# Performance work log

Hardware: AMD Instinct MI355X
Metric: run time of the kernel (lower is better)

The kernel has to match this reference:

```python
import jax, jax.numpy as jnp
import numpy as np

INF = 1.0e9
B, NI, NJ = 1, 768, 768
C_NODE, C_PAIR = 512, 128
H, C_HID = 8, 32
LN_EPS = 1e-5


def _ln(x, w, b):
    m = jnp.mean(x, axis=-1, keepdims=True)
    v = jnp.mean(jnp.square(x - m), axis=-1, keepdims=True)
    return (x - m) * jax.lax.rsqrt(v + LN_EPS) * w + b


def setup_inputs() -> dict:
    key = jax.random.key(0)
    ks = jax.random.split(key, 16)
    s_node = 1.0 / np.sqrt(C_NODE)
    s_pair = 1.0 / np.sqrt(C_PAIR)
    s_hid = 1.0 / np.sqrt(H * C_HID)
    inp = {
        "node_embed_i": jax.random.normal(ks[0], (B, NI, C_NODE), jnp.float32),
        "node_embed_j": jax.random.normal(ks[1], (B, NJ, C_NODE), jnp.float32),
        "pair_embed": jax.random.normal(ks[2], (B, NI, NJ, C_PAIR), jnp.float32),
        "pair_mask": (jax.random.uniform(ks[3], (B, NI, NJ)) < 0.95).astype(jnp.float32),
        "node_mask_i": (jax.random.uniform(ks[4], (B, NI)) < 0.98).astype(jnp.float32),
        # LayerNorm params
        "ln_i_w": jnp.ones((C_NODE,), jnp.float32), "ln_i_b": jnp.zeros((C_NODE,), jnp.float32),
        "ln_j_w": jnp.ones((C_NODE,), jnp.float32), "ln_j_b": jnp.zeros((C_NODE,), jnp.float32),
        "ln_p_w": jnp.ones((C_PAIR,), jnp.float32), "ln_p_b": jnp.zeros((C_PAIR,), jnp.float32),
        # pair-bias projection and its gate: Linear(C_PAIR, H)
        "W_pb": jax.random.normal(ks[5], (C_PAIR, H), jnp.float32) * s_pair,
        "b_pb": jnp.zeros((H,), jnp.float32),
        "W_pg": jax.random.normal(ks[6], (C_PAIR, H), jnp.float32) * s_pair,
        "b_pg": jnp.zeros((H,), jnp.float32),
        # attention projections (q/k/v bias-free, OpenFold-style)
        "Wq": jax.random.normal(ks[7], (C_NODE, H * C_HID), jnp.float32) * s_node,
        "Wk": jax.random.normal(ks[8], (C_NODE, H * C_HID), jnp.float32) * s_node,
        "Wv": jax.random.normal(ks[9], (C_NODE, H * C_HID), jnp.float32) * s_node,
        # output gate and output projection
        "Wg": jax.random.normal(ks[10], (C_NODE, H * C_HID), jnp.float32) * s_node,
        "bg": jnp.zeros((H * C_HID,), jnp.float32),
        "Wo": jax.random.normal(ks[11], (H * C_HID, C_NODE), jnp.float32) * s_hid,
        "bo": jnp.zeros((C_NODE,), jnp.float32),
    }
    return inp


def reference(node_embed_i, node_embed_j, pair_embed, pair_mask, node_mask_i,
              ln_i_w, ln_i_b, ln_j_w, ln_j_b, ln_p_w, ln_p_b,
              W_pb, b_pb, W_pg, b_pg, Wq, Wk, Wv, Wg, bg, Wo, bo):
    # LayerNorms
    qx = _ln(node_embed_i, ln_i_w, ln_i_b)           # [B,NI,C_NODE]
    kx = _ln(node_embed_j, ln_j_w, ln_j_b)           # [B,NJ,C_NODE]
    p = _ln(pair_embed, ln_p_w, ln_p_b)              # [B,NI,NJ,C_PAIR]

    # additive mask bias: 0 where valid, -inf where masked; broadcast over heads
    mask_bias = (INF * (pair_mask - 1.0))[:, None, :, :]          # [B,1,NI,NJ]

    # gated pair bias -> [B,H,NI,NJ] (permute_final_dims([2,0,1]))
    pb = (p @ W_pb + b_pb) * jax.nn.sigmoid(p @ W_pg + b_pg)      # [B,NI,NJ,H]
    pair_bias = jnp.transpose(pb, (0, 3, 1, 2))

    # multi-head attention with injected biases
    q = (qx @ Wq).reshape(B, NI, H, C_HID) * (C_HID ** -0.5)
    k = (kx @ Wk).reshape(B, NJ, H, C_HID)
    v = (kx @ Wv).reshape(B, NJ, H, C_HID)
    scores = jnp.einsum('bihc,bjhc->bhij', q, k) + mask_bias + pair_bias
    a = jax.nn.softmax(scores, axis=-1)                           # [B,H,NI,NJ]
    o = jnp.einsum('bhij,bjhc->bihc', a, v)                       # [B,NI,H,C_HID]

    # sigmoid output gate, flatten heads, output projection
    g = jax.nn.sigmoid(qx @ Wg + bg).reshape(B, NI, H, C_HID)
    o = (o * g).reshape(B, NI, H * C_HID)
    mha_out = o @ Wo + bo                                         # [B,NI,C_NODE]

    # residual on the layernormed input, scaled by node mask (dropout = identity at inference)
    return qx + mha_out * node_mask_i[..., None]
```

## Files before the change

kernel.cpp:

```cpp
#include <hip/hip_runtime.h>
#include <hip/hip_bf16.h>

#define NI 768
#define NJ 768
#define CN 512
#define CP 128
#define NH 8
#define CH 32
#define HC 256

typedef float  fx4  __attribute__((ext_vector_type(4)));
typedef float  fx2  __attribute__((ext_vector_type(2)));
typedef short  bv8  __attribute__((ext_vector_type(8)));
typedef unsigned short usx4 __attribute__((ext_vector_type(4)));

__device__ __forceinline__ short f2bf(float f) {
    __hip_bfloat16 h = __float2bfloat16(f);
    return *reinterpret_cast<short*>(&h);
}
__device__ __forceinline__ float bf2f(unsigned short u) {
    union { unsigned int u; float f; } c; c.u = ((unsigned int)u) << 16; return c.f;
}

__global__ __launch_bounds__(256) void fused_front_kernel(
    const float* __restrict__ node_i, const float* __restrict__ node_j,
    const float* __restrict__ ln_i_w, const float* __restrict__ ln_i_b,
    const float* __restrict__ ln_j_w, const float* __restrict__ ln_j_b,
    const float* __restrict__ Wq, const float* __restrict__ Wk,
    const float* __restrict__ Wv, const float* __restrict__ Wg,
    const float* __restrict__ bg,
    const float* __restrict__ lnpw, const float* __restrict__ lnpb,
    const float* __restrict__ Wpb, const float* __restrict__ bpb,
    const float* __restrict__ Wpg, const float* __restrict__ bpg,
    const float* __restrict__ pair, const float* __restrict__ pmask,
    float* __restrict__ qx, unsigned short* __restrict__ qsb,
    unsigned short* __restrict__ ksb, unsigned short* __restrict__ vtb,
    float* __restrict__ gs, unsigned short* __restrict__ biasb)
{
    const int bid = blockIdx.x;
    const int t = threadIdx.x;
    if (bid < 192) {
        __shared__ float xs[8][CN];
        __shared__ float red[4][8][2];
        const bool isj = bid >= 96;
        const int r0 = (isj ? bid - 96 : bid) * 8;
        const float* xin = isj ? node_j : node_i;
        const float* lw = isj ? ln_j_w : ln_i_w;
        const float* lb = isj ? ln_j_b : ln_i_b;
        const int wv = t >> 6;

        fx2 vrow[8]; float s8[8], q8[8];
#pragma unroll
        for (int r = 0; r < 8; ++r) {
            vrow[r] = *(const fx2*)(xin + (size_t)(r0 + r) * CN + t * 2);
            s8[r] = vrow[r][0] + vrow[r][1];
            q8[r] = vrow[r][0] * vrow[r][0] + vrow[r][1] * vrow[r][1];
        }
#pragma unroll
        for (int d = 1; d < 64; d <<= 1)
#pragma unroll
            for (int r = 0; r < 8; ++r) {
                s8[r] += __shfl_xor(s8[r], d);
                q8[r] += __shfl_xor(q8[r], d);
            }
        if ((t & 63) == 0)
#pragma unroll
            for (int r = 0; r < 8; ++r) { red[wv][r][0] = s8[r]; red[wv][r][1] = q8[r]; }
        __syncthreads();
        fx2 lwv = *(const fx2*)(lw + t * 2), lbv = *(const fx2*)(lb + t * 2);
#pragma unroll
        for (int r = 0; r < 8; ++r) {
            float s = red[0][r][0] + red[1][r][0] + red[2][r][0] + red[3][r][0];
            float q = red[0][r][1] + red[1][r][1] + red[2][r][1] + red[3][r][1];
            float mean = s * (1.f / CN);
            float var = q * (1.f / CN) - mean * mean;
            float rs = rsqrtf(var + 1e-5f);
            fx2 o;
            o[0] = (vrow[r][0] - mean) * rs * lwv[0] + lbv[0];
            o[1] = (vrow[r][1] - mean) * rs * lwv[1] + lbv[1];
            xs[r][t * 2] = o[0]; xs[r][t * 2 + 1] = o[1];
            if (!isj) *(fx2*)(qx + (size_t)(r0 + r) * CN + t * 2) = o;
        }
        __syncthreads();

        for (int m = 0; m < 2; ++m) {
            const float* W = isj ? (m ? Wv : Wk) : (m ? Wg : Wq);
            float acc[8] = {0.f,0.f,0.f,0.f,0.f,0.f,0.f,0.f};
            for (int cc = 0; cc < CN; cc += 4) {
                fx4 xv[8];
#pragma unroll
                for (int r = 0; r < 8; ++r) xv[r] = *(const fx4*)&xs[r][cc];
#pragma unroll
                for (int u = 0; u < 4; ++u) {
                    float w = W[(size_t)(cc + u) * HC + t];
#pragma unroll
                    for (int r = 0; r < 8; ++r) acc[r] = fmaf(xv[r][u], w, acc[r]);
                }
            }
            if (!isj) {
                if (m == 0) {
#pragma unroll
                    for (int r = 0; r < 8; ++r)
                        qsb[(size_t)(r0 + r) * HC + t] =
                            (unsigned short)f2bf(acc[r] * 0.17677669529663687f);
                } else {
#pragma unroll
                    for (int r = 0; r < 8; ++r)
                        gs[(size_t)(r0 + r) * HC + t] =
                            1.f / (1.f + __expf(-(acc[r] + bg[t])));
                }
            } else {
                if (m == 0) {
#pragma unroll
                    for (int r = 0; r < 8; ++r)
                        ksb[(size_t)(r0 + r) * HC + t] = (unsigned short)f2bf(acc[r]);
                } else {
                    bv8 vv;
#pragma unroll
                    for (int r = 0; r < 8; ++r) vv[r] = f2bf(acc[r]);
                    *(bv8*)&vtb[(size_t)t * NJ + r0] = vv;
                }
            }
        }
        return;
    }

    __shared__ unsigned short wcatT[16][136];
    __shared__ float redS[16][16], redC[16][16];
    __shared__ float scalS[16], scalC[16];
    __shared__ unsigned short sb[8][68];

    const int lane = t & 63;
    const int wave = t >> 6;
    const int bid2 = bid - 192;
    const int i    = bid2 / 12;
    const int jt64 = (bid2 % 12) * 64;
    const int jt   = jt64 + wave * 16;
    const int o  = lane & 15;
    const int kq = lane >> 4;

    const float* prow = pair + ((size_t)i * NJ + (jt + o)) * CP + kq * 8;
    fx4 x0[4], x1[4];
#pragma unroll
    for (int s = 0; s < 4; ++s) {
        x0[s] = *(const fx4*)(prow + s * 32);
        x1[s] = *(const fx4*)(prow + s * 32 + 4);
    }

    {
        const int oo = t & 15, cg = t >> 4;
        float pS = 0.f, pC = 0.f;
#pragma unroll
        for (int e = 0; e < 8; ++e) {
            int c = cg * 8 + e;
            float w = (oo < 8) ? Wpb[c * 8 + oo] : Wpg[c * 8 + (oo - 8)];
            float wv = lnpw[c] * w;
            short b = f2bf(wv);
            wcatT[oo][c] = (unsigned short)b;
            pS += bf2f((unsigned short)b);
            pC += lnpb[c] * w;
        }
        redS[cg][oo] = pS; redC[cg][oo] = pC;
        __syncthreads();
        if (t < 16) {
            float s = 0.f, c2 = 0.f;
#pragma unroll
            for (int k = 0; k < 16; ++k) { s += redS[k][t]; c2 += redC[k][t]; }
            scalS[t] = s;
            scalC[t] = c2 + ((t < 8) ? bpb[t] : bpg[t - 8]);
        }
        __syncthreads();
    }

    bv8 bfrag[4];
#pragma unroll
    for (int s = 0; s < 4; ++s)
        bfrag[s] = *(const bv8*)&wcatT[o][s * 32 + kq * 8];
    const float spb = scalS[o];
    const float cpb = scalC[o];

    bv8 afrag[4];
#pragma unroll
    for (int s = 0; s < 4; ++s) {
#pragma unroll
        for (int u = 0; u < 4; ++u) {
            afrag[s][u]     = f2bf(x0[s][u]);
            afrag[s][u + 4] = f2bf(x1[s][u]);
        }
    }
    bv8 ones;
#pragma unroll
    for (int u = 0; u < 8; ++u) ones[u] = (short)0x3F80;

    fx4 acc  = {0.f, 0.f, 0.f, 0.f};
    fx4 accS = {0.f, 0.f, 0.f, 0.f};
    fx4 accG = {0.f, 0.f, 0.f, 0.f};
#pragma unroll
    for (int s = 0; s < 4; ++s) {
        acc  = __builtin_amdgcn_mfma_f32_16x16x32_bf16(afrag[s], bfrag[s], acc,  0, 0, 0);
        accS = __builtin_amdgcn_mfma_f32_16x16x32_bf16(afrag[s], ones,     accS, 0, 0, 0);
        accG = __builtin_amdgcn_mfma_f32_16x16x32_bf16(afrag[s], afrag[s], accG, 0, 0, 0);
    }

#pragma unroll
    for (int r = 0; r < 4; ++r) {
        const int p = kq * 4 + r;
        float sp = accS[r];
        float qp = __shfl(accG[r], kq * 20 + r);
        float mean = sp * (1.f / CP);
        float var  = qp * (1.f / CP) - mean * mean;
        float rstd = rsqrtf(var + 1e-5f);
        float pre  = rstd * (acc[r] - mean * spb) + cpb;
        float part = __shfl_xor(pre, 8);
        if (o < 8) {
            float sig = 1.f / (1.f + __expf(-part));
            int j = jt + p;
            float b = pre * sig + (pmask[(size_t)i * NJ + j] - 1.f) * 1.0e9f;
            sb[o][wave * 16 + p] = (unsigned short)f2bf(b);
        }
    }
    __syncthreads();
    if (t < 128) {
        const int oo = t >> 4, ck = t & 15;
        usx4 v;
#pragma unroll
        for (int u = 0; u < 4; ++u) v[u] = sb[oo][ck * 4 + u];
        *(usx4*)&biasb[((size_t)oo * NI + i) * NJ + jt64 + ck * 4] = v;
    }
}

__global__ __launch_bounds__(256) void attn_kernel(
    const short* __restrict__ qsb, const short* __restrict__ ksb,
    const short* __restrict__ vtb, const unsigned short* __restrict__ biasb,
    float* __restrict__ pnum, float* __restrict__ pden)
{
    __shared__ unsigned short P[32][392];
    __shared__ float sumbuf[4][32];
    const int i0 = blockIdx.x * 32;
    const int h  = blockIdx.y;
    const int jh = blockIdx.z;
    const int jbase = jh * 384;
    const int pb = ((int)blockIdx.x * NH + h) * 2 + jh;
    const int t = threadIdx.x;
    const int w = t >> 6;
    const int lane = t & 63;
    const int rowl = lane & 15;
    const int g = lane >> 4;

    bv8 aq[2];
#pragma unroll
    for (int it = 0; it < 2; ++it)
        aq[it] = *(const bv8*)&qsb[(size_t)(i0 + it * 16 + rowl) * HC + h * CH + g * 8];

    const unsigned short* bbase = biasb + (size_t)h * NI * NJ;
    float rs[2][4] = {{0.f,0.f,0.f,0.f},{0.f,0.f,0.f,0.f}};
    for (int jt = 0; jt < 6; ++jt) {
        const int jloc = w * 96 + jt * 16;
        const int jb = jbase + jloc;
        bv8 bk = *(const bv8*)&ksb[(size_t)(jb + rowl) * HC + h * CH + g * 8];
#pragma unroll
        for (int it = 0; it < 2; ++it) {
            fx4 acc = {0.f, 0.f, 0.f, 0.f};
            acc = __builtin_amdgcn_mfma_f32_16x16x32_bf16(aq[it], bk, acc, 0, 0, 0);
#pragma unroll
            for (int r = 0; r < 4; ++r) {
                const int il = it * 16 + g * 4 + r;
                float s = acc[r] + bf2f(bbase[(size_t)(i0 + il) * NJ + jb + rowl]);
                float p = __expf(s);
                rs[it][r] += p;
                P[il][jloc + rowl] = (unsigned short)f2bf(p);
            }
        }
    }
#pragma unroll
    for (int it = 0; it < 2; ++it)
#pragma unroll
        for (int r = 0; r < 4; ++r) {
            float v = rs[it][r];
            v += __shfl_xor(v, 1); v += __shfl_xor(v, 2);
            v += __shfl_xor(v, 4); v += __shfl_xor(v, 8);
            rs[it][r] = v;
        }
    if (rowl == 0) {
#pragma unroll
        for (int it = 0; it < 2; ++it)
#pragma unroll
            for (int r = 0; r < 4; ++r)
                sumbuf[w][it * 16 + g * 4 + r] = rs[it][r];
    }
    __syncthreads();

    if (t < 32)
        pden[(size_t)pb * 32 + t] =
            sumbuf[0][t] + sumbuf[1][t] + sumbuf[2][t] + sumbuf[3][t];

    const int it = w & 1, ct = w >> 1;
    fx4 acc = {0.f, 0.f, 0.f, 0.f};
    for (int kk = 0; kk < 12; ++kk) {
        const int jloc = kk * 32;
        bv8 ap = *(const bv8*)&P[it * 16 + rowl][jloc + g * 8];
        bv8 bv = *(const bv8*)&vtb[(size_t)(h * CH + ct * 16 + rowl) * NJ + jbase + jloc + g * 8];
        acc = __builtin_amdgcn_mfma_f32_16x16x32_bf16(ap, bv, acc, 0, 0, 0);
    }
#pragma unroll
    for (int r = 0; r < 4; ++r) {
        const int il = it * 16 + g * 4 + r;
        pnum[(size_t)pb * 1024 + il * 32 + ct * 16 + rowl] = acc[r];
    }
}

__global__ __launch_bounds__(256) void combine_out_kernel(
    const float* __restrict__ pnum, const float* __restrict__ pden,
    const float* __restrict__ gs, const float* __restrict__ qx,
    const float* __restrict__ Wo, const float* __restrict__ bo,
    const float* __restrict__ mi, float* __restrict__ outp)
{
    __shared__ float ogl[2][HC];
    const int r0 = blockIdx.x * 2;
    const int t = threadIdx.x;
    const int h = t >> 5, c = t & 31;
#pragma unroll
    for (int r = 0; r < 2; ++r) {
        const int i = r0 + r;
        const int pb = ((i >> 5) * NH + h) * 2;
        const int il = i & 31;
        float n = pnum[(size_t)(pb + 0) * 1024 + il * 32 + c]
                + pnum[(size_t)(pb + 1) * 1024 + il * 32 + c];
        float d = pden[(size_t)(pb + 0) * 32 + il]
                + pden[(size_t)(pb + 1) * 32 + il];
        ogl[r][t] = n / d * gs[(size_t)i * HC + t];
    }
    __syncthreads();

    float acc[2][2] = {{0,0},{0,0}};
    for (int cc = 0; cc < HC; cc += 4) {
        fx4 xr0 = *(const fx4*)&ogl[0][cc];
        fx4 xr1 = *(const fx4*)&ogl[1][cc];
#pragma unroll
        for (int u = 0; u < 4; ++u) {
            float w0 = Wo[(size_t)(cc + u) * CN + t];
            float w1 = Wo[(size_t)(cc + u) * CN + 256 + t];
            acc[0][0] = fmaf(xr0[u], w0, acc[0][0]); acc[0][1] = fmaf(xr0[u], w1, acc[0][1]);
            acc[1][0] = fmaf(xr1[u], w0, acc[1][0]); acc[1][1] = fmaf(xr1[u], w1, acc[1][1]);
        }
    }
#pragma unroll
    for (int r = 0; r < 2; ++r) {
        float mk = mi[r0 + r];
        size_t base = (size_t)(r0 + r) * CN;
        outp[base + t]       = qx[base + t]       + (acc[r][0] + bo[t])       * mk;
        outp[base + 256 + t] = qx[base + 256 + t] + (acc[r][1] + bo[t + 256]) * mk;
    }
}

extern "C" void kernel_launch(void* const* d_in, const int* in_sizes, int n_in,
                              void* d_out, int out_size, void* d_ws, size_t ws_size,
                              hipStream_t stream)
{
    const float* node_i = (const float*)d_in[0];
    const float* node_j = (const float*)d_in[1];
    const float* pair   = (const float*)d_in[2];
    const float* pmask  = (const float*)d_in[3];
    const float* nmask  = (const float*)d_in[4];
    const float* ln_i_w = (const float*)d_in[5];
    const float* ln_i_b = (const float*)d_in[6];
    const float* ln_j_w = (const float*)d_in[7];
    const float* ln_j_b = (const float*)d_in[8];
    const float* ln_p_w = (const float*)d_in[9];
    const float* ln_p_b = (const float*)d_in[10];
    const float* W_pb   = (const float*)d_in[11];
    const float* b_pb   = (const float*)d_in[12];
    const float* W_pg   = (const float*)d_in[13];
    const float* b_pg   = (const float*)d_in[14];
    const float* Wq     = (const float*)d_in[15];
    const float* Wk     = (const float*)d_in[16];
    const float* Wv     = (const float*)d_in[17];
    const float* Wg     = (const float*)d_in[18];
    const float* bg     = (const float*)d_in[19];
    const float* Wo     = (const float*)d_in[20];
    const float* bo     = (const float*)d_in[21];
    float* outp = (float*)d_out;

    float* fw = (float*)d_ws;
    float* qx   = fw;
    float* gs   = qx + (size_t)NI * CN;
    float* pnum = gs + (size_t)NI * HC;
    float* pden = pnum + (size_t)24 * NH * 2 * 1024;
    unsigned short* qsb = (unsigned short*)(pden + (size_t)24 * NH * 2 * 32);
    unsigned short* ksb = qsb + (size_t)NI * HC;
    unsigned short* vtb = ksb + (size_t)NJ * HC;
    unsigned short* biasb = vtb + (size_t)HC * NJ;

    hipLaunchKernelGGL(fused_front_kernel, dim3(192 + (NI * NJ) / 64), dim3(256), 0, stream,
                       node_i, node_j, ln_i_w, ln_i_b, ln_j_w, ln_j_b,
                       Wq, Wk, Wv, Wg, bg,
                       ln_p_w, ln_p_b, W_pb, b_pb, W_pg, b_pg,
                       pair, pmask,
                       qx, qsb, ksb, vtb, gs, biasb);
    hipLaunchKernelGGL(attn_kernel, dim3(NI / 32, NH, 2), dim3(256), 0, stream,
                       (const short*)qsb, (const short*)ksb, (const short*)vtb,
                       biasb, pnum, pden);
    hipLaunchKernelGGL(combine_out_kernel, dim3(NI / 2), dim3(256), 0, stream,
                       pnum, pden, gs, qx, Wo, bo, nmask, outp);
}
```

Baseline: 108.9 us.

## Split attention key dimension into six chunks and preload K, bias, V tiles

The attention kernel now splits the key dimension into six 128-wide slices instead of two 384-wide halves, tripling the grid to expose more parallelism. Each block preloads its K fragments, bias values and V fragments into registers before computation, so global loads are issued early and overlap. The combine kernel sums six partial numerators and denominators instead of two. The cost is larger partial-result workspace, more reduction reads, and higher register pressure.

```diff
diff --git a/kernel.cpp b/kernel.cpp
--- a/kernel.cpp
+++ b/kernel.cpp
@@ -8,6 +8,8 @@
 #define NH 8
 #define CH 32
 #define HC 256
+#define NSTR 6
+#define SJ 128
 
 typedef float  fx4  __attribute__((ext_vector_type(4)));
 typedef float  fx2  __attribute__((ext_vector_type(2)));
@@ -234,13 +236,12 @@
     const short* __restrict__ vtb, const unsigned short* __restrict__ biasb,
     float* __restrict__ pnum, float* __restrict__ pden)
 {
-    __shared__ unsigned short P[32][392];
+    __shared__ unsigned short P[32][136];
     __shared__ float sumbuf[4][32];
     const int i0 = blockIdx.x * 32;
     const int h  = blockIdx.y;
-    const int jh = blockIdx.z;
-    const int jbase = jh * 384;
-    const int pb = ((int)blockIdx.x * NH + h) * 2 + jh;
+    const int jbase = blockIdx.z * SJ;
+    const int pb = ((int)blockIdx.x * NH + h) * NSTR + blockIdx.z;
     const int t = threadIdx.x;
     const int w = t >> 6;
     const int lane = t & 63;
@@ -252,20 +253,38 @@
     for (int it = 0; it < 2; ++it)
         aq[it] = *(const bv8*)&qsb[(size_t)(i0 + it * 16 + rowl) * HC + h * CH + g * 8];
 
+    bv8 bk[2];
+#pragma unroll
+    for (int jt = 0; jt < 2; ++jt) {
+        const int jb = jbase + w * 32 + jt * 16;
+        bk[jt] = *(const bv8*)&ksb[(size_t)(jb + rowl) * HC + h * CH + g * 8];
+    }
     const unsigned short* bbase = biasb + (size_t)h * NI * NJ;
+    unsigned short bl[2][2][4];
+#pragma unroll
+    for (int jt = 0; jt < 2; ++jt) {
+        const int jb = jbase + w * 32 + jt * 16;
+#pragma unroll
+        for (int it = 0; it < 2; ++it)
+#pragma unroll
+            for (int r = 0; r < 4; ++r) {
+                const int il = it * 16 + g * 4 + r;
+                bl[jt][it][r] = bbase[(size_t)(i0 + il) * NJ + jb + rowl];
+            }
+    }
+
     float rs[2][4] = {{0.f,0.f,0.f,0.f},{0.f,0.f,0.f,0.f}};
-    for (int jt = 0; jt < 6; ++jt) {
-        const int jloc = w * 96 + jt * 16;
-        const int jb = jbase + jloc;
-        bv8 bk = *(const bv8*)&ksb[(size_t)(jb + rowl) * HC + h * CH + g * 8];
+#pragma unroll
+    for (int jt = 0; jt < 2; ++jt) {
+        const int jloc = w * 32 + jt * 16;
 #pragma unroll
         for (int it = 0; it < 2; ++it) {
             fx4 acc = {0.f, 0.f, 0.f, 0.f};
-            acc = __builtin_amdgcn_mfma_f32_16x16x32_bf16(aq[it], bk, acc, 0, 0, 0);
+            acc = __builtin_amdgcn_mfma_f32_16x16x32_bf16(aq[it], bk[jt], acc, 0, 0, 0);
 #pragma unroll
             for (int r = 0; r < 4; ++r) {
                 const int il = it * 16 + g * 4 + r;
-                float s = acc[r] + bf2f(bbase[(size_t)(i0 + il) * NJ + jb + rowl]);
+                float s = acc[r] + bf2f(bl[jt][it][r]);
                 float p = __expf(s);
                 rs[it][r] += p;
                 P[il][jloc + rowl] = (unsigned short)f2bf(p);
@@ -288,19 +307,24 @@
             for (int r = 0; r < 4; ++r)
                 sumbuf[w][it * 16 + g * 4 + r] = rs[it][r];
     }
+
+    const int it = w & 1, ct = w >> 1;
+    bv8 vv[4];
+#pragma unroll
+    for (int kk = 0; kk < 4; ++kk)
+        vv[kk] = *(const bv8*)&vtb[(size_t)(h * CH + ct * 16 + rowl) * NJ + jbase + kk * 32 + g * 8];
+
     __syncthreads();
 
     if (t < 32)
         pden[(size_t)pb * 32 + t] =
             sumbuf[0][t] + sumbuf[1][t] + sumbuf[2][t] + sumbuf[3][t];
 
-    const int it = w & 1, ct = w >> 1;
     fx4 acc = {0.f, 0.f, 0.f, 0.f};
-    for (int kk = 0; kk < 12; ++kk) {
-        const int jloc = kk * 32;
-        bv8 ap = *(const bv8*)&P[it * 16 + rowl][jloc + g * 8];
-        bv8 bv = *(const bv8*)&vtb[(size_t)(h * CH + ct * 16 + rowl) * NJ + jbase + jloc + g * 8];
-        acc = __builtin_amdgcn_mfma_f32_16x16x32_bf16(ap, bv, acc, 0, 0, 0);
+#pragma unroll
+    for (int kk = 0; kk < 4; ++kk) {
+        bv8 ap = *(const bv8*)&P[it * 16 + rowl][kk * 32 + g * 8];
+        acc = __builtin_amdgcn_mfma_f32_16x16x32_bf16(ap, vv[kk], acc, 0, 0, 0);
     }
 #pragma unroll
     for (int r = 0; r < 4; ++r) {
@@ -322,12 +346,14 @@
 #pragma unroll
     for (int r = 0; r < 2; ++r) {
         const int i = r0 + r;
-        const int pb = ((i >> 5) * NH + h) * 2;
+        const int pb = ((i >> 5) * NH + h) * NSTR;
         const int il = i & 31;
-        float n = pnum[(size_t)(pb + 0) * 1024 + il * 32 + c]
-                + pnum[(size_t)(pb + 1) * 1024 + il * 32 + c];
-        float d = pden[(size_t)(pb + 0) * 32 + il]
-                + pden[(size_t)(pb + 1) * 32 + il];
+        float n = 0.f, d = 0.f;
+#pragma unroll
+        for (int s = 0; s < NSTR; ++s) {
+            n += pnum[(size_t)(pb + s) * 1024 + il * 32 + c];
+            d += pden[(size_t)(pb + s) * 32 + il];
+        }
         ogl[r][t] = n / d * gs[(size_t)i * HC + t];
     }
     __syncthreads();
@@ -385,8 +411,8 @@
     float* qx   = fw;
     float* gs   = qx + (size_t)NI * CN;
     float* pnum = gs + (size_t)NI * HC;
-    float* pden = pnum + (size_t)24 * NH * 2 * 1024;
-    unsigned short* qsb = (unsigned short*)(pden + (size_t)24 * NH * 2 * 32);
+    float* pden = pnum + (size_t)24 * NH * NSTR * 1024;
+    unsigned short* qsb = (unsigned short*)(pden + (size_t)24 * NH * NSTR * 32);
     unsigned short* ksb = qsb + (size_t)NI * HC;
     unsigned short* vtb = ksb + (size_t)NJ * HC;
     unsigned short* biasb = vtb + (size_t)HC * NJ;
@@ -397,7 +423,7 @@
                        ln_p_w, ln_p_b, W_pb, b_pb, W_pg, b_pg,
                        pair, pmask,
                        qx, qsb, ksb, vtb, gs, biasb);
-    hipLaunchKernelGGL(attn_kernel, dim3(NI / 32, NH, 2), dim3(256), 0, stream,
+    hipLaunchKernelGGL(attn_kernel, dim3(NI / 32, NH, NSTR), dim3(256), 0, stream,
                        (const short*)qsb, (const short*)ksb, (const short*)vtb,
                        biasb, pnum, pden);
     hipLaunchKernelGGL(combine_out_kernel, dim3(NI / 2), dim3(256), 0, stream,
```

Result: no change. 110.0 us (+1.0%).
